# Kernel tuning notes

Measured on AMD Instinct MI355X. Metric: run time of the kernel, lower is better.

The kernel has to match this reference:

```python
import jax, jax.numpy as jnp
import numpy as np

# Module config (matches init_kwargs)
T, B, C = 2048, 8, 1024   # seq_len, batch, input_size
H, K = 16, 31             # num_heads, kernel_size
PAD_L = 30                # padding_l (causal)


def setup_inputs() -> dict:
    key = jax.random.key(0)
    k1, k2 = jax.random.split(key)
    x = jax.random.normal(k1, (T, B, C), dtype=jnp.float32)
    # nn.Parameter(num_heads, kernel_size), xavier-init approximated by randn
    weight = jax.random.normal(k2, (H, K), dtype=jnp.float32)
    return {"x": x, "weight": weight}


def reference(x, weight):
    # x: (T, B, C); weight: (H, K)
    # weight_softmax=True: softmax over kernel taps per head
    w = jax.nn.softmax(weight, axis=-1)  # (H, K)
    # permute to (B, C, T) as the CUDA kernel expects
    x_bct = jnp.transpose(x, (1, 2, 0))
    # expand per-head kernel to per-channel depthwise kernel: (C, 1, K)
    w_ck = jnp.repeat(w, C // H, axis=0)[:, None, :]
    # lightconv: out[b,c,t] = sum_k w[head(c),k] * x_pad[b,c,t+k],
    # left pad = PAD_L, right pad = K-1-PAD_L (causal when PAD_L=K-1).
    # conv_general_dilated is cross-correlation, matching the CUDA kernel.
    out = jax.lax.conv_general_dilated(
        x_bct, w_ck,
        window_strides=(1,),
        padding=[(PAD_L, K - 1 - PAD_L)],
        dimension_numbers=("NCH", "OIH", "NCH"),
        feature_group_count=C,
    )  # (B, C, T)
    # bias=False, so just permute back to (T, B, C)
    return jnp.transpose(out, (2, 0, 1))
```

## Files before the change

### kernel.cpp

```cpp
#include <hip/hip_runtime.h>
#include <math.h>

#define T_LEN 2048
#define B_SZ  8
#define C_SZ  1024
#define NH    16
#define KW    31
#define HALO  (KW - 1)
#define TT    8
#define CHUNK 128
#define NTILE (CHUNK / TT)
#define RING  64
#define WIN   (TT + HALO)
#define ROWSTRIDE (B_SZ * C_SZ)

#define GLOBAL_AS(p) ((const __attribute__((address_space(1))) void*)(p))
#define LDS_AS(p)    ((__attribute__((address_space(3))) void*)(p))

__global__ __launch_bounds__(64, 2) void lightconv_kernel(
    const float* __restrict__ x, const float* __restrict__ weight,
    float* __restrict__ out) {
  __shared__ float ring[RING][64];
  const int lane = threadIdx.x;

  const int cgrp = blockIdx.x & 15;
  const int tc   = blockIdx.x >> 4;
  const int b    = blockIdx.y;
  const int c0   = cgrp * 64;
  const int tb   = tc * CHUNK;

  float wv[KW];
  float m = -1e30f;
#pragma unroll
  for (int k = 0; k < KW; ++k) {
    wv[k] = weight[cgrp * KW + k];
    m = fmaxf(m, wv[k]);
  }
  float s = 0.f;
#pragma unroll
  for (int k = 0; k < KW; ++k) {
    wv[k] = expf(wv[k] - m);
    s += wv[k];
  }
  const float inv = 1.f / s;
  float wk[KW];
#pragma unroll
  for (int k = 0; k < KW; ++k) {
    wk[k] = __uint_as_float(
        __builtin_amdgcn_readfirstlane(__float_as_uint(wv[k] * inv)));
  }

  const float* xbase = x + (size_t)b * C_SZ + c0;
  const int lane_off = (lane >> 4) * ROWSTRIDE + (lane & 15) * 4;

  if (tb == 0) {
#pragma unroll
    for (int i = 0; i < 32; ++i) ring[32 + i][lane] = 0.f;
#pragma unroll
    for (int r4 = 0; r4 < 2; ++r4) {
      const float* gp = xbase + (size_t)(r4 * 4) * ROWSTRIDE + lane_off;
      __builtin_amdgcn_global_load_lds(GLOBAL_AS(gp),
                                       LDS_AS(&ring[r4 * 4][0]), 16, 0, 0);
    }
  } else {
#pragma unroll
    for (int r4 = 0; r4 < 10; ++r4) {
      const float* gp = xbase + (size_t)(tb - 32 + r4 * 4) * ROWSTRIDE + lane_off;
      __builtin_amdgcn_global_load_lds(GLOBAL_AS(gp),
                                       LDS_AS(&ring[(32 + 4 * r4) & (RING - 1)][0]),
                                       16, 0, 0);
    }
  }
#pragma unroll
  for (int r4 = 0; r4 < 2; ++r4) {
    const float* gp = xbase + (size_t)(tb + TT + r4 * 4) * ROWSTRIDE + lane_off;
    __builtin_amdgcn_global_load_lds(GLOBAL_AS(gp),
                                     LDS_AS(&ring[8 + r4 * 4][0]), 16, 0, 0);
  }

#pragma unroll 1
  for (int jo = 0; jo < 2; ++jo) {
#pragma unroll
    for (int jj = 0; jj < NTILE / 2; ++jj) {
      const int j = jo * 8 + jj;
      const int tstart = tb + jo * 64 + jj * TT;

      if (j <= NTILE - 3) {
#pragma unroll
        for (int r4 = 0; r4 < 2; ++r4) {
          const float* gp =
              xbase + (size_t)(tstart + 2 * TT + r4 * 4) * ROWSTRIDE + lane_off;
          __builtin_amdgcn_global_load_lds(
              GLOBAL_AS(gp),
              LDS_AS(&ring[(8 * jj + 16 + r4 * 4) & (RING - 1)][0]), 16, 0, 0);
        }
      }
      if (j == 0)                asm volatile("s_waitcnt vmcnt(4)"  ::: "memory");
      else if (j == 1)           asm volatile("s_waitcnt vmcnt(12)" ::: "memory");
      else if (j == NTILE - 2)   asm volatile("s_waitcnt vmcnt(18)" ::: "memory");
      else if (j == NTILE - 1)   asm volatile("s_waitcnt vmcnt(16)" ::: "memory");
      else                       asm volatile("s_waitcnt vmcnt(20)" ::: "memory");
      __builtin_amdgcn_sched_barrier(0);

      float xv[WIN];
#pragma unroll
      for (int i = 0; i < WIN; ++i) {
        xv[i] = ring[(8 * jj + i + 34) & (RING - 1)][lane];
      }
      float* op = out + ((size_t)tstart * B_SZ + b) * C_SZ + c0 + lane;
#pragma unroll
      for (int o = 0; o < TT; ++o) {
        float a = 0.f;
#pragma unroll
        for (int k = 0; k < KW; ++k) a = fmaf(wk[k], xv[o + k], a);
        op[(size_t)o * ROWSTRIDE] = a;
      }
    }
  }
}

extern "C" void kernel_launch(void* const* d_in, const int* in_sizes, int n_in,
                              void* d_out, int out_size, void* d_ws, size_t ws_size,
                              hipStream_t stream) {
  const float* x = (const float*)d_in[0];
  const float* w = (const float*)d_in[1];
  float* out = (float*)d_out;
  (void)in_sizes; (void)n_in; (void)out_size; (void)d_ws; (void)ws_size;

  dim3 grid((C_SZ / 64) * (T_LEN / CHUNK), B_SZ);
  dim3 block(64);
  lightconv_kernel<<<grid, block, 0, stream>>>(x, w, out);
}
```

Measured before the change: 30.80 us.

## Widen blocks to four waves sharing a 256-channel LDS ring buffer

Each block now covers 256 channels (four heads) with four wavefronts instead of one wave per 64 channels. Each wave issues full contiguous 1 KB row loads into a shared LDS ring rather than four partial rows, so global accesses per row become wider and more contiguous. Because waves now read rows loaded by other waves, workgroup barriers are added after the prologue and before each tile's ring reads. The grid shrinks fourfold, which cuts per-block overhead but adds barrier synchronisation and may lower latency hiding because waves stall together.

```diff
diff --git a/kernel.cpp b/kernel.cpp
--- a/kernel.cpp
+++ b/kernel.cpp
@@ -12,28 +12,32 @@
 #define NTILE (CHUNK / TT)
 #define RING  64
 #define WIN   (TT + HALO)
+#define CG    256
 #define ROWSTRIDE (B_SZ * C_SZ)
 
 #define GLOBAL_AS(p) ((const __attribute__((address_space(1))) void*)(p))
 #define LDS_AS(p)    ((__attribute__((address_space(3))) void*)(p))
 
-__global__ __launch_bounds__(64, 2) void lightconv_kernel(
+__global__ __launch_bounds__(256, 2) void lightconv_kernel(
     const float* __restrict__ x, const float* __restrict__ weight,
     float* __restrict__ out) {
-  __shared__ float ring[RING][64];
-  const int lane = threadIdx.x;
+  __shared__ float ring[RING][CG];
+  const int tid  = threadIdx.x;
+  const int w    = tid >> 6;
+  const int lane = tid & 63;
 
-  const int cgrp = blockIdx.x & 15;
-  const int tc   = blockIdx.x >> 4;
-  const int b    = blockIdx.y;
-  const int c0   = cgrp * 64;
-  const int tb   = tc * CHUNK;
+  const int cg = blockIdx.x & 3;
+  const int tc = blockIdx.x >> 2;
+  const int b  = blockIdx.y;
+  const int c0 = cg * CG;
+  const int tb = tc * CHUNK;
 
+  const int head = cg * 4 + w;
   float wv[KW];
   float m = -1e30f;
 #pragma unroll
   for (int k = 0; k < KW; ++k) {
-    wv[k] = weight[cgrp * KW + k];
+    wv[k] = weight[head * KW + k];
     m = fmaxf(m, wv[k]);
   }
   float s = 0.f;
@@ -51,32 +55,39 @@
   }
 
   const float* xbase = x + (size_t)b * C_SZ + c0;
-  const int lane_off = (lane >> 4) * ROWSTRIDE + (lane & 15) * 4;
+  const int loff = lane * 4;
 
   if (tb == 0) {
 #pragma unroll
-    for (int i = 0; i < 32; ++i) ring[32 + i][lane] = 0.f;
+    for (int i = 0; i < 32; ++i) ring[32 + i][tid] = 0.f;
 #pragma unroll
-    for (int r4 = 0; r4 < 2; ++r4) {
-      const float* gp = xbase + (size_t)(r4 * 4) * ROWSTRIDE + lane_off;
-      __builtin_amdgcn_global_load_lds(GLOBAL_AS(gp),
-                                       LDS_AS(&ring[r4 * 4][0]), 16, 0, 0);
+    for (int pp = 0; pp < 2; ++pp) {
+      const int t = w + 4 * pp;
+      const float* gp = xbase + (size_t)t * ROWSTRIDE + loff;
+      __builtin_amdgcn_global_load_lds(GLOBAL_AS(gp), LDS_AS(&ring[t][0]),
+                                       16, 0, 0);
     }
   } else {
 #pragma unroll
-    for (int r4 = 0; r4 < 10; ++r4) {
-      const float* gp = xbase + (size_t)(tb - 32 + r4 * 4) * ROWSTRIDE + lane_off;
-      __builtin_amdgcn_global_load_lds(GLOBAL_AS(gp),
-                                       LDS_AS(&ring[(32 + 4 * r4) & (RING - 1)][0]),
+    for (int pp = 0; pp < 10; ++pp) {
+      const int t = tb - 32 + w + 4 * pp;
+      const int slot = (32 + w + 4 * pp) & (RING - 1);
+      const float* gp = xbase + (size_t)t * ROWSTRIDE + loff;
+      __builtin_amdgcn_global_load_lds(GLOBAL_AS(gp), LDS_AS(&ring[slot][0]),
                                        16, 0, 0);
     }
   }
 #pragma unroll
-  for (int r4 = 0; r4 < 2; ++r4) {
-    const float* gp = xbase + (size_t)(tb + TT + r4 * 4) * ROWSTRIDE + lane_off;
-    __builtin_amdgcn_global_load_lds(GLOBAL_AS(gp),
-                                     LDS_AS(&ring[8 + r4 * 4][0]), 16, 0, 0);
+  for (int pp = 0; pp < 2; ++pp) {
+    const int t = tb + TT + w + 4 * pp;
+    const int slot = 8 + w + 4 * pp;
+    const float* gp = xbase + (size_t)t * ROWSTRIDE + loff;
+    __builtin_amdgcn_global_load_lds(GLOBAL_AS(gp), LDS_AS(&ring[slot][0]),
+                                     16, 0, 0);
   }
+  asm volatile("s_waitcnt vmcnt(2) lgkmcnt(0)" ::: "memory");
+  __builtin_amdgcn_s_barrier();
+  __builtin_amdgcn_sched_barrier(0);
 
 #pragma unroll 1
   for (int jo = 0; jo < 2; ++jo) {
@@ -87,12 +98,12 @@
 
       if (j <= NTILE - 3) {
 #pragma unroll
-        for (int r4 = 0; r4 < 2; ++r4) {
-          const float* gp =
-              xbase + (size_t)(tstart + 2 * TT + r4 * 4) * ROWSTRIDE + lane_off;
-          __builtin_amdgcn_global_load_lds(
-              GLOBAL_AS(gp),
-              LDS_AS(&ring[(8 * jj + 16 + r4 * 4) & (RING - 1)][0]), 16, 0, 0);
+        for (int pp = 0; pp < 2; ++pp) {
+          const int t = tstart + 2 * TT + w + 4 * pp;
+          const int slot = (8 * jj + 16 + w + 4 * pp) & (RING - 1);
+          const float* gp = xbase + (size_t)t * ROWSTRIDE + loff;
+          __builtin_amdgcn_global_load_lds(GLOBAL_AS(gp),
+                                           LDS_AS(&ring[slot][0]), 16, 0, 0);
         }
       }
       if (j == 0)                asm volatile("s_waitcnt vmcnt(4)"  ::: "memory");
@@ -101,13 +112,15 @@
       else if (j == NTILE - 1)   asm volatile("s_waitcnt vmcnt(16)" ::: "memory");
       else                       asm volatile("s_waitcnt vmcnt(20)" ::: "memory");
       __builtin_amdgcn_sched_barrier(0);
+      __builtin_amdgcn_s_barrier();
+      __builtin_amdgcn_sched_barrier(0);
 
       float xv[WIN];
 #pragma unroll
       for (int i = 0; i < WIN; ++i) {
-        xv[i] = ring[(8 * jj + i + 34) & (RING - 1)][lane];
+        xv[i] = ring[(8 * jj + 34 + i) & (RING - 1)][tid];
       }
-      float* op = out + ((size_t)tstart * B_SZ + b) * C_SZ + c0 + lane;
+      float* op = out + ((size_t)tstart * B_SZ + b) * C_SZ + c0 + tid;
 #pragma unroll
       for (int o = 0; o < TT; ++o) {
         float a = 0.f;
@@ -127,7 +140,7 @@
   float* out = (float*)d_out;
   (void)in_sizes; (void)n_in; (void)out_size; (void)d_ws; (void)ws_size;
 
-  dim3 grid((C_SZ / 64) * (T_LEN / CHUNK), B_SZ);
-  dim3 block(64);
+  dim3 grid((C_SZ / CG) * (T_LEN / CHUNK), B_SZ);
+  dim3 block(256);
   lightconv_kernel<<<grid, block, 0, stream>>>(x, w, out);
 }
```

Result: slower. 32.77 us (+6.4%).

## Keep convolution halo in registers as a sliding window and halve the time chunk

Applied to the files above, without the earlier changes.

The 30-row halo now lives in registers and slides forward after each 8-row tile. Each tile copies only the 8 new rows from an LDS ring, which shrinks to 32 rows. The time chunk per block drops from 128 to 64 and launch bounds request 4 blocks per CU, giving more parallelism and occupancy. The cost is a larger share of redundant halo reads, now issued as scalar-width global loads. The hand-tuned vmcnt waits are kept unchanged, so correct ordering depends on loads and stores still being counted the way those values assume.

```diff
diff --git a/kernel.cpp b/kernel.cpp
--- a/kernel.cpp
+++ b/kernel.cpp
@@ -8,16 +8,16 @@
 #define KW    31
 #define HALO  (KW - 1)
 #define TT    8
-#define CHUNK 128
+#define CHUNK 64
 #define NTILE (CHUNK / TT)
-#define RING  64
+#define RING  32
 #define WIN   (TT + HALO)
 #define ROWSTRIDE (B_SZ * C_SZ)
 
 #define GLOBAL_AS(p) ((const __attribute__((address_space(1))) void*)(p))
 #define LDS_AS(p)    ((__attribute__((address_space(3))) void*)(p))
 
-__global__ __launch_bounds__(64, 2) void lightconv_kernel(
+__global__ __launch_bounds__(64, 4) void lightconv_kernel(
     const float* __restrict__ x, const float* __restrict__ weight,
     float* __restrict__ out) {
   __shared__ float ring[RING][64];
@@ -53,69 +53,58 @@
   const float* xbase = x + (size_t)b * C_SZ + c0;
   const int lane_off = (lane >> 4) * ROWSTRIDE + (lane & 15) * 4;
 
+  float xv[WIN];
   if (tb == 0) {
 #pragma unroll
-    for (int i = 0; i < 32; ++i) ring[32 + i][lane] = 0.f;
-#pragma unroll
-    for (int r4 = 0; r4 < 2; ++r4) {
-      const float* gp = xbase + (size_t)(r4 * 4) * ROWSTRIDE + lane_off;
-      __builtin_amdgcn_global_load_lds(GLOBAL_AS(gp),
-                                       LDS_AS(&ring[r4 * 4][0]), 16, 0, 0);
-    }
+    for (int i = 0; i < HALO; ++i) xv[i] = 0.f;
   } else {
 #pragma unroll
-    for (int r4 = 0; r4 < 10; ++r4) {
-      const float* gp = xbase + (size_t)(tb - 32 + r4 * 4) * ROWSTRIDE + lane_off;
-      __builtin_amdgcn_global_load_lds(GLOBAL_AS(gp),
-                                       LDS_AS(&ring[(32 + 4 * r4) & (RING - 1)][0]),
-                                       16, 0, 0);
+    for (int i = 0; i < HALO; ++i) {
+      xv[i] = xbase[(size_t)(tb - HALO + i) * ROWSTRIDE + lane];
     }
   }
 #pragma unroll
-  for (int r4 = 0; r4 < 2; ++r4) {
-    const float* gp = xbase + (size_t)(tb + TT + r4 * 4) * ROWSTRIDE + lane_off;
-    __builtin_amdgcn_global_load_lds(GLOBAL_AS(gp),
-                                     LDS_AS(&ring[8 + r4 * 4][0]), 16, 0, 0);
+  for (int r4 = 0; r4 < 4; ++r4) {
+    const float* gp = xbase + (size_t)(tb + 4 * r4) * ROWSTRIDE + lane_off;
+    __builtin_amdgcn_global_load_lds(GLOBAL_AS(gp), LDS_AS(&ring[4 * r4][0]),
+                                     16, 0, 0);
   }
 
-#pragma unroll 1
-  for (int jo = 0; jo < 2; ++jo) {
 #pragma unroll
-    for (int jj = 0; jj < NTILE / 2; ++jj) {
-      const int j = jo * 8 + jj;
-      const int tstart = tb + jo * 64 + jj * TT;
+  for (int j = 0; j < NTILE; ++j) {
+    const int tstart = tb + j * TT;
 
-      if (j <= NTILE - 3) {
+    if (j <= NTILE - 3) {
 #pragma unroll
-        for (int r4 = 0; r4 < 2; ++r4) {
-          const float* gp =
-              xbase + (size_t)(tstart + 2 * TT + r4 * 4) * ROWSTRIDE + lane_off;
-          __builtin_amdgcn_global_load_lds(
-              GLOBAL_AS(gp),
-              LDS_AS(&ring[(8 * jj + 16 + r4 * 4) & (RING - 1)][0]), 16, 0, 0);
-        }
-      }
-      if (j == 0)                asm volatile("s_waitcnt vmcnt(4)"  ::: "memory");
-      else if (j == 1)           asm volatile("s_waitcnt vmcnt(12)" ::: "memory");
-      else if (j == NTILE - 2)   asm volatile("s_waitcnt vmcnt(18)" ::: "memory");
-      else if (j == NTILE - 1)   asm volatile("s_waitcnt vmcnt(16)" ::: "memory");
-      else                       asm volatile("s_waitcnt vmcnt(20)" ::: "memory");
-      __builtin_amdgcn_sched_barrier(0);
-
-      float xv[WIN];
-#pragma unroll
-      for (int i = 0; i < WIN; ++i) {
-        xv[i] = ring[(8 * jj + i + 34) & (RING - 1)][lane];
-      }
-      float* op = out + ((size_t)tstart * B_SZ + b) * C_SZ + c0 + lane;
-#pragma unroll
-      for (int o = 0; o < TT; ++o) {
-        float a = 0.f;
-#pragma unroll
-        for (int k = 0; k < KW; ++k) a = fmaf(wk[k], xv[o + k], a);
-        op[(size_t)o * ROWSTRIDE] = a;
+      for (int r4 = 0; r4 < 2; ++r4) {
+        const float* gp =
+            xbase + (size_t)(tstart + 2 * TT + 4 * r4) * ROWSTRIDE + lane_off;
+        __builtin_amdgcn_global_load_lds(
+            GLOBAL_AS(gp), LDS_AS(&ring[(8 * j + 16 + 4 * r4) & (RING - 1)][0]),
+            16, 0, 0);
       }
     }
+    if (j == 0)                asm volatile("s_waitcnt vmcnt(4)"  ::: "memory");
+    else if (j == 1)           asm volatile("s_waitcnt vmcnt(12)" ::: "memory");
+    else if (j == NTILE - 2)   asm volatile("s_waitcnt vmcnt(18)" ::: "memory");
+    else if (j == NTILE - 1)   asm volatile("s_waitcnt vmcnt(16)" ::: "memory");
+    else                       asm volatile("s_waitcnt vmcnt(20)" ::: "memory");
+    __builtin_amdgcn_sched_barrier(0);
+
+#pragma unroll
+    for (int i = 0; i < TT; ++i) {
+      xv[HALO + i] = ring[(8 * j + i) & (RING - 1)][lane];
+    }
+    float* op = out + ((size_t)tstart * B_SZ + b) * C_SZ + c0 + lane;
+#pragma unroll
+    for (int o = 0; o < TT; ++o) {
+      float a = 0.f;
+#pragma unroll
+      for (int k = 0; k < KW; ++k) a = fmaf(wk[k], xv[o + k], a);
+      op[(size_t)o * ROWSTRIDE] = a;
+    }
+#pragma unroll
+    for (int i = 0; i < HALO; ++i) xv[i] = xv[i + TT];
   }
 }
 
```

Result: slower. 33.14 us (+7.6%).
